# Optimization experiments

Measured on AMD Instinct MI355X. Metric: run time of the kernel, lower is better.

Reference implementation:

```python
import jax, jax.numpy as jnp
import numpy as np

HIDDEN = 4096
NUM_HEADS = 32
HEAD_DIM = HIDDEN // NUM_HEADS
B, S = 2, 2048
ROPE_BASE = 10000.0


def setup_inputs() -> dict:
    key = jax.random.key(0)
    k1, k2, k3, k4 = jax.random.split(key, 4)
    hidden_states = jax.random.normal(k1, (B, S, HIDDEN), dtype=jnp.float32)
    positions = jnp.tile(jnp.arange(S, dtype=jnp.int32)[None, :], (B, 1))
    W_qkv = jax.random.normal(k2, (HIDDEN, 3 * HIDDEN), dtype=jnp.float32) * (HIDDEN ** -0.5)
    b_qkv = jax.random.normal(k3, (3 * HIDDEN,), dtype=jnp.float32) * 0.02
    W_o = jax.random.normal(k4, (HIDDEN, HIDDEN), dtype=jnp.float32) * (HIDDEN ** -0.5)
    return {"hidden_states": hidden_states, "positions": positions,
            "W_qkv": W_qkv, "b_qkv": b_qkv, "W_o": W_o}


def _rope(x, positions):
    # x: [B, S, H, D]; GPT-NeoX style full-dim rotary (rotary_dim = head_dim)
    half = HEAD_DIM // 2
    inv_freq = 1.0 / (ROPE_BASE ** (jnp.arange(0, half, dtype=jnp.float32) * 2.0 / HEAD_DIM))
    ang = positions.astype(jnp.float32)[:, :, None] * inv_freq[None, None, :]  # [B,S,half]
    cos = jnp.cos(ang)[:, :, None, :]  # [B,S,1,half]
    sin = jnp.sin(ang)[:, :, None, :]
    x1, x2 = x[..., :half], x[..., half:]
    return jnp.concatenate([x1 * cos - x2 * sin, x2 * cos + x1 * sin], axis=-1)


def reference(hidden_states, positions, W_qkv, b_qkv, W_o):
    qkv = jnp.einsum('bsh,hk->bsk', hidden_states, W_qkv) + b_qkv
    q, k, v = jnp.split(qkv, 3, axis=-1)
    q = q.reshape(B, S, NUM_HEADS, HEAD_DIM)
    k = k.reshape(B, S, NUM_HEADS, HEAD_DIM)
    v = v.reshape(B, S, NUM_HEADS, HEAD_DIM)
    q = _rope(q, positions)
    k = _rope(k, positions)
    scale = HEAD_DIM ** -0.5
    scores = jnp.einsum('bqhd,bkhd->bhqk', q, k) * scale  # [B,H,S,S]
    causal = jnp.tril(jnp.ones((S, S), dtype=bool))
    scores = jnp.where(causal[None, None], scores, jnp.float32(-1e30))
    probs = jax.nn.softmax(scores, axis=-1)
    ctx = jnp.einsum('bhqk,bkhd->bqhd', probs, v).reshape(B, S, HIDDEN)
    return jnp.einsum('bsh,ho->bso', ctx, W_o)
```

## Files before the change

### kernel.cpp

```cpp
#include <hip/hip_runtime.h>
#include <stdint.h>

#define HID 4096
#define NHD 32
#define HD  128
#define BB  2
#define SS  2048
#define BSZ (BB*SS)
#define N3  (3*HID)

typedef __bf16 bf16x8 __attribute__((ext_vector_type(8)));
typedef __bf16 bf16x4 __attribute__((ext_vector_type(4)));
typedef float  f32x4  __attribute__((ext_vector_type(4)));

#define MFMA16(A,B,C) __builtin_amdgcn_mfma_f32_16x16x32_bf16((A),(B),(C),0,0,0)

__device__ __forceinline__ void gl_lds16(const __bf16* g, __bf16* l) {
  __builtin_amdgcn_global_load_lds(
      (__attribute__((address_space(1))) void*)g,
      (__attribute__((address_space(3))) void*)l, 16, 0, 0);
}

__global__ void cvt_bf16(const float* __restrict__ in, __bf16* __restrict__ out, int n) {
  int i = (blockIdx.x * blockDim.x + threadIdx.x) * 4;
  if (i >= n) return;
  float4 v = *(const float4*)(in + i);
  bf16x4 r;
  r[0] = (__bf16)v.x; r[1] = (__bf16)v.y; r[2] = (__bf16)v.z; r[3] = (__bf16)v.w;
  *(bf16x4*)(out + i) = r;
}

__global__ void transp_cvt(const float* __restrict__ in, __bf16* __restrict__ out,
                           int R, int C) {
  __shared__ float t[64 * 65];
  int c0 = blockIdx.x * 64, r0 = blockIdx.y * 64;
  int tx = threadIdx.x & 15, ty = threadIdx.x >> 4;
  for (int j = 0; j < 4; ++j) {
    float4 v = *(const float4*)(in + (size_t)(r0 + ty + 16 * j) * C + c0 + tx * 4);
    float* d = t + (ty + 16 * j) * 65 + tx * 4;
    d[0] = v.x; d[1] = v.y; d[2] = v.z; d[3] = v.w;
  }
  __syncthreads();
  for (int j = 0; j < 4; ++j) {
    int cc = ty + 16 * j;
    bf16x4 o4;
    for (int e = 0; e < 4; ++e) o4[e] = (__bf16)t[(tx * 4 + e) * 65 + cc];
    *(bf16x4*)(out + (size_t)(c0 + cc) * R + r0 + tx * 4) = o4;
  }
}

__global__ __launch_bounds__(256, 2) void gemm_qkv(
    const __bf16* __restrict__ A, const __bf16* __restrict__ Bt,
    const float* __restrict__ bias, const int* __restrict__ pos,
    __bf16* __restrict__ qr, __bf16* __restrict__ kr, __bf16* __restrict__ vt,
    int M, int N, int K) {
  const int TS = 146;
  __shared__ __bf16 smem[128 * TS];
  __bf16* sA = smem;
  __bf16* sB = smem + 4096;
  const int tid = threadIdx.x;
  const int wave = tid >> 6, lane = tid & 63;
  const int quad = lane >> 4, l15 = lane & 15;
  const int t = blockIdx.y * gridDim.x + blockIdx.x;
  const int grp = t / (16 * gridDim.x), rem = t % (16 * gridDim.x);
  const int m0 = (grp * 16 + (rem & 15)) * 128;
  const int n0 = (rem >> 4) * 128;
  const int wm = (wave >> 1) * 64, wn = (wave & 1) * 64;

  f32x4 acc[4][4];
  for (int i = 0; i < 4; ++i)
    for (int j = 0; j < 4; ++j)
      acc[i][j] = (f32x4){0.f, 0.f, 0.f, 0.f};

  for (int k0 = 0; k0 < K; k0 += 32) {
    __syncthreads();
    for (int i = 0; i < 2; ++i) {
      int off = tid * 16 + i * 4096;
      int r = off >> 6;
      int c = (off >> 4) & 3;
      int cs = c ^ ((r >> 1) & 3);
      gl_lds16(A  + (size_t)(m0 + r) * K + k0 + cs * 8, sA + (off >> 1));
      gl_lds16(Bt + (size_t)(n0 + r) * K + k0 + cs * 8, sB + (off >> 1));
    }
    __syncthreads();
    bf16x8 af[4], bf[4];
    for (int i = 0; i < 4; ++i) {
      int ra = wm + i * 16 + l15;
      int rb = wn + i * 16 + l15;
      af[i] = *(const bf16x8*)(sA + ra * 32 + (quad ^ ((ra >> 1) & 3)) * 8);
      bf[i] = *(const bf16x8*)(sB + rb * 32 + (quad ^ ((rb >> 1) & 3)) * 8);
    }
    for (int im = 0; im < 4; ++im)
      for (int in = 0; in < 4; ++in)
        acc[im][in] = MFMA16(af[im], bf[in], acc[im][in]);
  }

  __syncthreads();
  for (int im = 0; im < 4; ++im)
    for (int in = 0; in < 4; ++in) {
      int col = wn + in * 16 + l15;
      float bv = bias[n0 + col];
      for (int r = 0; r < 4; ++r)
        smem[(wm + im * 16 + quad * 4 + r) * TS + col] =
            (__bf16)(acc[im][in][r] + bv);
    }
  __syncthreads();

  const int reg = n0 >> 12;
  const int h   = (n0 & 4095) >> 7;
  const int b   = m0 >> 11;
  const int s0  = m0 & 2047;
  const int bh  = b * NHD + h;

  if (reg == 2) {
    __bf16* dst = vt + (size_t)bh * HD * SS;
    int l16 = tid & 15, cb = tid >> 4;
    for (int p = 0; p < 8; ++p) {
      int c = cb + 16 * p;
      bf16x8 v8;
      for (int e = 0; e < 8; ++e) v8[e] = smem[(l16 * 8 + e) * TS + c];
      *(bf16x8*)(dst + (size_t)c * SS + s0 + l16 * 8) = v8;
    }
  } else {
    __bf16* dst = (reg == 0 ? qr : kr) + (size_t)bh * SS * HD;
    const float osc = (reg == 0) ? 0.08838834764831845f : 1.0f;
    int d2 = tid & 63, rb = (tid >> 6) * 32;
    float freq = expf(-0.14391156831212787f * (float)d2);
    for (int i = 0; i < 32; ++i) {
      int r = rb + i;
      float p = (float)pos[b * SS + s0 + r];
      float sn, cs;
      sincosf(p * freq, &sn, &cs);
      float x1 = (float)smem[r * TS + d2];
      float x2 = (float)smem[r * TS + d2 + 64];
      dst[(size_t)(s0 + r) * HD + d2]      = (__bf16)((x1 * cs - x2 * sn) * osc);
      dst[(size_t)(s0 + r) * HD + d2 + 64] = (__bf16)((x2 * cs + x1 * sn) * osc);
    }
  }
}

__global__ __launch_bounds__(256, 2) void gemm_bt(
    const __bf16* __restrict__ A, const __bf16* __restrict__ Bt,
    float* __restrict__ Cout, int M, int N, int K) {
  __shared__ __bf16 sA[128 * 32];
  __shared__ __bf16 sB[128 * 32];
  const int tid = threadIdx.x;
  const int wave = tid >> 6, lane = tid & 63;
  const int quad = lane >> 4, l15 = lane & 15;
  const int t = blockIdx.y * gridDim.x + blockIdx.x;
  const int grp = t / (16 * gridDim.x), rem = t % (16 * gridDim.x);
  const int m0 = (grp * 16 + (rem & 15)) * 128;
  const int n0 = (rem >> 4) * 128;
  const int wm = (wave >> 1) * 64, wn = (wave & 1) * 64;

  f32x4 acc[4][4];
  for (int i = 0; i < 4; ++i)
    for (int j = 0; j < 4; ++j)
      acc[i][j] = (f32x4){0.f, 0.f, 0.f, 0.f};

  for (int k0 = 0; k0 < K; k0 += 32) {
    __syncthreads();
    for (int i = 0; i < 2; ++i) {
      int off = tid * 16 + i * 4096;
      int r = off >> 6;
      int c = (off >> 4) & 3;
      int cs = c ^ ((r >> 1) & 3);
      gl_lds16(A  + (size_t)(m0 + r) * K + k0 + cs * 8, sA + (off >> 1));
      gl_lds16(Bt + (size_t)(n0 + r) * K + k0 + cs * 8, sB + (off >> 1));
    }
    __syncthreads();
    bf16x8 af[4], bf[4];
    for (int i = 0; i < 4; ++i) {
      int ra = wm + i * 16 + l15;
      int rb = wn + i * 16 + l15;
      af[i] = *(const bf16x8*)(sA + ra * 32 + (quad ^ ((ra >> 1) & 3)) * 8);
      bf[i] = *(const bf16x8*)(sB + rb * 32 + (quad ^ ((rb >> 1) & 3)) * 8);
    }
    for (int im = 0; im < 4; ++im)
      for (int in = 0; in < 4; ++in)
        acc[im][in] = MFMA16(af[im], bf[in], acc[im][in]);
  }

  for (int im = 0; im < 4; ++im)
    for (int in = 0; in < 4; ++in) {
      int col = n0 + wn + in * 16 + l15;
      for (int r = 0; r < 4; ++r) {
        int row = m0 + wm + im * 16 + quad * 4 + r;
        Cout[(size_t)row * N + col] = acc[im][in][r];
      }
    }
}

__global__ __launch_bounds__(256, 2) void flash_attn(
    const __bf16* __restrict__ qr, const __bf16* __restrict__ kr,
    const __bf16* __restrict__ vt, __bf16* __restrict__ ctx) {
  __shared__ __bf16 sKP[4 * 32 * 136];
  __shared__ __bf16 sV[128 * 128];
  const int bh = blockIdx.x;
  const int qt = 15 - blockIdx.y;
  const int b = bh >> 5, h = bh & 31;
  const int tid = threadIdx.x;
  const int wave = tid >> 6, lane = tid & 63;
  const int quad = lane >> 4, l15 = lane & 15;
  const int q0 = qt * 128;

  const __bf16* qbase = qr + (size_t)bh * SS * HD;
  const __bf16* kbase = kr + (size_t)bh * SS * HD;
  const __bf16* vbase = vt + (size_t)bh * HD * SS;
  __bf16* sK = sKP;
  __bf16* pw = sKP + wave * (32 * 136);

  bf16x8 qf[2][4];
  for (int im = 0; im < 2; ++im) {
    int row = q0 + wave * 32 + im * 16 + l15;
    for (int ks = 0; ks < 4; ++ks)
      qf[im][ks] = *(const bf16x8*)(qbase + (size_t)row * HD + ks * 32 + quad * 8);
  }

  f32x4 o[2][8];
  for (int im = 0; im < 2; ++im)
    for (int jd = 0; jd < 8; ++jd)
      o[im][jd] = (f32x4){0.f, 0.f, 0.f, 0.f};
  float l_i[2][4];
  for (int im = 0; im < 2; ++im)
    for (int rg = 0; rg < 4; ++rg) l_i[im][rg] = 0.f;

  for (int kt = 0; kt <= qt; ++kt) {
    const int k0 = kt * 128;
    __syncthreads();
    for (int i = 0; i < 8; ++i) {
      int off = tid * 16 + i * 4096;
      int r  = off >> 8;
      int cl = (off >> 4) & 15;
      int cg = (cl & 8) | ((cl & 7) ^ (r & 7));
      gl_lds16(kbase + (size_t)(k0 + r) * HD + cg * 8, sK + (off >> 1));
      gl_lds16(vbase + (size_t)r * SS + k0 + cg * 8,   sV + (off >> 1));
    }
    __syncthreads();

    f32x4 s[2][8];
    for (int im = 0; im < 2; ++im)
      for (int jn = 0; jn < 8; ++jn)
        s[im][jn] = (f32x4){0.f, 0.f, 0.f, 0.f};
    for (int ks = 0; ks < 4; ++ks) {
      bf16x8 kf[8];
      for (int jn = 0; jn < 8; ++jn) {
        int row = jn * 16 + l15;
        int c = ks * 4 + quad;
        int p = (c & 8) | ((c & 7) ^ (row & 7));
        kf[jn] = *(const bf16x8*)(sK + row * 128 + p * 8);
      }
      for (int im = 0; im < 2; ++im)
        for (int jn = 0; jn < 8; ++jn)
          s[im][jn] = MFMA16(qf[im][ks], kf[jn], s[im][jn]);
    }
    __syncthreads();

    const bool diag = (kt == qt);
    for (int im = 0; im < 2; ++im)
      for (int rg = 0; rg < 4; ++rg) {
        int rowg = q0 + wave * 32 + im * 16 + quad * 4 + rg;
        float rs = 0.f;
        for (int jn = 0; jn < 8; ++jn) {
          float p = (diag && (k0 + jn * 16 + l15) > rowg)
                        ? 0.f : __expf(s[im][jn][rg]);
          s[im][jn][rg] = p;
          rs += p;
        }
        for (int d = 1; d < 16; d <<= 1) rs += __shfl_xor(rs, d);
        l_i[im][rg] += rs;
      }

    for (int im = 0; im < 2; ++im)
      for (int jn = 0; jn < 8; ++jn)
        for (int rg = 0; rg < 4; ++rg)
          pw[(im * 16 + quad * 4 + rg) * 136 + jn * 16 + l15] =
              (__bf16)s[im][jn][rg];

    for (int ks = 0; ks < 4; ++ks) {
      bf16x8 pf[2], vf[8];
      for (int im = 0; im < 2; ++im)
        pf[im] = *(const bf16x8*)(pw + (im * 16 + l15) * 136 + ks * 32 + quad * 8);
      for (int jd = 0; jd < 8; ++jd) {
        int row = jd * 16 + l15;
        int c = ks * 4 + quad;
        int p = (c & 8) | ((c & 7) ^ (row & 7));
        vf[jd] = *(const bf16x8*)(sV + row * 128 + p * 8);
      }
      for (int im = 0; im < 2; ++im)
        for (int jd = 0; jd < 8; ++jd)
          o[im][jd] = MFMA16(pf[im], vf[jd], o[im][jd]);
    }
  }

  __bf16* cb = ctx + (size_t)(b * SS) * HID + h * HD;
  for (int im = 0; im < 2; ++im)
    for (int rg = 0; rg < 4; ++rg) {
      float inv = 1.0f / l_i[im][rg];
      int row = q0 + wave * 32 + im * 16 + quad * 4 + rg;
      for (int jd = 0; jd < 8; ++jd)
        cb[(size_t)row * HID + jd * 16 + l15] = (__bf16)(o[im][jd][rg] * inv);
    }
}

extern "C" void kernel_launch(void* const* d_in, const int* in_sizes, int n_in,
                              void* d_out, int out_size, void* d_ws, size_t ws_size,
                              hipStream_t stream) {
  const float* hs   = (const float*)d_in[0];
  const int*   pos  = (const int*)d_in[1];
  const float* Wqkv = (const float*)d_in[2];
  const float* bqkv = (const float*)d_in[3];
  const float* Wo   = (const float*)d_in[4];

  char* ws = (char*)d_ws;
  const size_t M32 = 33554432;
  __bf16* hsb   = (__bf16*)(ws);
  __bf16* wqkvT = (__bf16*)(ws + M32);
  __bf16* woT   = (__bf16*)(ws + 4 * M32);
  __bf16* qr    = (__bf16*)(ws + 5 * M32);
  __bf16* kr    = (__bf16*)(ws + 6 * M32);
  __bf16* vt    = (__bf16*)(ws + 7 * M32);
  __bf16* ctx   = hsb;

  cvt_bf16<<<(BSZ * HID) / 1024, 256, 0, stream>>>(hs, hsb, BSZ * HID);
  transp_cvt<<<dim3(N3 / 64, HID / 64), 256, 0, stream>>>(Wqkv, wqkvT, HID, N3);
  transp_cvt<<<dim3(HID / 64, HID / 64), 256, 0, stream>>>(Wo, woT, HID, HID);
  gemm_qkv<<<dim3(N3 / 128, BSZ / 128), 256, 0, stream>>>(hsb, wqkvT, bqkv, pos,
                                                          qr, kr, vt, BSZ, N3, HID);
  flash_attn<<<dim3(BB * NHD, SS / 128), 256, 0, stream>>>(qr, kr, vt, ctx);
  gemm_bt<<<dim3(HID / 128, BSZ / 128), 256, 0, stream>>>(ctx, woT, (float*)d_out,
                                                          BSZ, HID, HID);
}
```

Measured before the change: 1.170 ms.

## Rewrite GEMMs as 256x256 tiles with double-buffered 8-wave pipelined core

Both projection GEMMs move from 128x128 tiles with a K-step of 32 and two syncs per step to a shared 256x256-tile core. The core uses 512 threads, K-steps of 64 and double-buffered LDS, and interleaves global-to-LDS prefetch with MFMA phases using explicit barriers, waitcnt control and setprio. The block index is remapped with a simple swizzle for L2 locality, and the QKV epilogue is adapted to the larger tile with a new LDS swizzle. This targets load latency stalls and low arithmetic intensity. The cost is 128KB of LDS per block and very high register pressure, which may cap occupancy at one block per CU despite the launch bounds.

After: 964.8 us. 1.21x faster.

```diff
diff --git a/kernel.cpp b/kernel.cpp
--- a/kernel.cpp
+++ b/kernel.cpp
@@ -20,6 +20,16 @@
       (__attribute__((address_space(1))) void*)g,
       (__attribute__((address_space(3))) void*)l, 16, 0, 0);
 }
+
+__device__ __forceinline__ void block_bar() {
+  __builtin_amdgcn_sched_barrier(0);
+  __builtin_amdgcn_s_barrier();
+  __builtin_amdgcn_sched_barrier(0);
+}
+#define LGKM0() do { asm volatile("s_waitcnt lgkmcnt(0)" ::: "memory"); \
+                     __builtin_amdgcn_sched_barrier(0); } while (0)
+#define VMC(n)  do { asm volatile("s_waitcnt vmcnt(" #n ")" ::: "memory"); \
+                     __builtin_amdgcn_sched_barrier(0); } while (0)
 
 __global__ void cvt_bf16(const float* __restrict__ in, __bf16* __restrict__ out, int n) {
   int i = (blockIdx.x * blockDim.x + threadIdx.x) * 4;
@@ -49,146 +59,248 @@
   }
 }
 
-__global__ __launch_bounds__(256, 2) void gemm_qkv(
+
+__device__ __forceinline__ void ld_a4(bf16x8 a[4][2], const __bf16* base, int row, int quad) {
+#pragma unroll
+  for (int m = 0; m < 4; ++m) {
+    const int rr = row + m * 16;
+    const int sw = rr & 7;
+#pragma unroll
+    for (int kk = 0; kk < 2; ++kk)
+      a[m][kk] = *(const bf16x8*)(base + rr * 64 + ((kk * 4 + quad) ^ sw) * 8);
+  }
+}
+__device__ __forceinline__ void ld_b2(bf16x8 b[2][2], const __bf16* base, int row, int quad) {
+#pragma unroll
+  for (int n = 0; n < 2; ++n) {
+    const int rr = row + n * 16;
+    const int sw = rr & 7;
+#pragma unroll
+    for (int kk = 0; kk < 2; ++kk)
+      b[n][kk] = *(const bf16x8*)(base + rr * 64 + ((kk * 4 + quad) ^ sw) * 8);
+  }
+}
+__device__ __forceinline__ void mma_quad(f32x4 acc[8][4], bf16x8 a[4][2],
+                                         bf16x8 b[2][2], int mh, int nh) {
+  __builtin_amdgcn_s_setprio(1);
+#pragma unroll
+  for (int m = 0; m < 4; ++m)
+#pragma unroll
+    for (int n = 0; n < 2; ++n) {
+      f32x4 c = acc[mh * 4 + m][nh * 2 + n];
+      c = MFMA16(a[m][0], b[n][0], c);
+      c = MFMA16(a[m][1], b[n][1], c);
+      acc[mh * 4 + m][nh * 2 + n] = c;
+    }
+  __builtin_amdgcn_s_setprio(0);
+}
+
+__device__ __forceinline__ void core256(const __bf16* __restrict__ Ab,
+                                        const __bf16* __restrict__ Bb,
+                                        int K, __bf16* smem, f32x4 acc[8][4]) {
+  const int tid  = threadIdx.x;
+  const int wave = tid >> 6, lane = tid & 63;
+  const int quad = lane >> 4, l15 = lane & 15;
+  const int arow = ((wave >> 2) * 64) + l15;
+  const int brow = ((wave & 3) * 32) + l15;
+  const int NKT = K >> 6, NIT = NKT >> 1;
+
+  __bf16* aBuf[2] = { smem,          smem + 16384 };
+  __bf16* bBuf[2] = { smem + 32768,  smem + 49152 };
+
+  const int off0 = tid * 16, off1 = off0 + 8192;
+  const int r0 = off0 >> 7, r1 = off1 >> 7;
+  const int sO0 = r0 * K + ((((off0 >> 4) & 7) ^ (r0 & 7)) * 8);
+  const int sO1 = r1 * K + ((((off1 >> 4) & 7) ^ (r1 & 7)) * 8);
+  const int d0 = off0 >> 1, d1 = off1 >> 1;
+
+#define STG_A(buf, half, kt) do { \
+    const __bf16* s_ = Ab + (size_t)(half) * 128 * K + (size_t)(kt) * 64; \
+    gl_lds16(s_ + sO0, aBuf[buf] + (half) * 8192 + d0); \
+    gl_lds16(s_ + sO1, aBuf[buf] + (half) * 8192 + d1); } while (0)
+#define STG_B(buf, half, kt) do { \
+    const __bf16* s_ = Bb + (size_t)(half) * 128 * K + (size_t)(kt) * 64; \
+    gl_lds16(s_ + sO0, bBuf[buf] + (half) * 8192 + d0); \
+    gl_lds16(s_ + sO1, bBuf[buf] + (half) * 8192 + d1); } while (0)
+
+  bf16x8 a_r[4][2], bn0[2][2], bn1[2][2];
+
+  STG_A(0, 0, 0); STG_B(0, 0, 0); STG_B(0, 1, 0); STG_A(0, 1, 0);
+  STG_A(1, 0, 1); STG_B(1, 0, 1); STG_B(1, 1, 1);
+  VMC(6);
+  block_bar();
+
+  for (int i = 0; i < NIT; ++i) {
+    const bool last = (i == NIT - 1);
+    const int t1 = 2 * i + 1, t2 = 2 * i + 2, t3 = 2 * i + 3;
+
+    ld_a4(a_r, aBuf[0],        arow, quad);
+    ld_b2(bn0, bBuf[0],        brow, quad);
+    STG_A(1, 1, t1);
+    block_bar(); LGKM0();
+    mma_quad(acc, a_r, bn0, 0, 0);
+    block_bar();
+
+    ld_b2(bn1, bBuf[0] + 8192, brow, quad);
+    if (!last) STG_A(0, 0, t2);
+    block_bar(); LGKM0();
+    mma_quad(acc, a_r, bn1, 0, 1);
+    block_bar();
+
+    ld_a4(a_r, aBuf[0] + 8192, arow, quad);
+    if (!last) STG_B(0, 0, t2);
+    block_bar(); LGKM0();
+    mma_quad(acc, a_r, bn1, 1, 1);
+    block_bar();
+
+    if (!last) STG_B(0, 1, t2);
+    block_bar();
+    mma_quad(acc, a_r, bn0, 1, 0);
+    if (last) { VMC(0); } else { VMC(6); }
+    block_bar();
+
+    ld_a4(a_r, aBuf[1],        arow, quad);
+    ld_b2(bn0, bBuf[1],        brow, quad);
+    if (!last) STG_A(0, 1, t2);
+    block_bar(); LGKM0();
+    mma_quad(acc, a_r, bn0, 0, 0);
+    block_bar();
+
+    ld_b2(bn1, bBuf[1] + 8192, brow, quad);
+    if (!last) STG_A(1, 0, t3);
+    block_bar(); LGKM0();
+    mma_quad(acc, a_r, bn1, 0, 1);
+    block_bar();
+
+    ld_a4(a_r, aBuf[1] + 8192, arow, quad);
+    if (!last) STG_B(1, 0, t3);
+    block_bar(); LGKM0();
+    mma_quad(acc, a_r, bn1, 1, 1);
+    block_bar();
+
+    if (!last) STG_B(1, 1, t3);
+    block_bar();
+    mma_quad(acc, a_r, bn0, 1, 0);
+    VMC(6);
+    block_bar();
+  }
+#undef STG_A
+#undef STG_B
+}
+
+__device__ __forceinline__ int eswz(int r, int c) {
+  return r * 256 + ((((c >> 3) ^ (r & 31) ^ (r >> 5)) & 31) * 8) + (c & 7);
+}
+
+__global__ __launch_bounds__(512, 2) void gemm_qkv(
     const __bf16* __restrict__ A, const __bf16* __restrict__ Bt,
     const float* __restrict__ bias, const int* __restrict__ pos,
     __bf16* __restrict__ qr, __bf16* __restrict__ kr, __bf16* __restrict__ vt,
     int M, int N, int K) {
-  const int TS = 146;
-  __shared__ __bf16 smem[128 * TS];
-  __bf16* sA = smem;
-  __bf16* sB = smem + 4096;
+  __shared__ __bf16 smem[65536];
   const int tid = threadIdx.x;
   const int wave = tid >> 6, lane = tid & 63;
   const int quad = lane >> 4, l15 = lane & 15;
-  const int t = blockIdx.y * gridDim.x + blockIdx.x;
-  const int grp = t / (16 * gridDim.x), rem = t % (16 * gridDim.x);
-  const int m0 = (grp * 16 + (rem & 15)) * 128;
-  const int n0 = (rem >> 4) * 128;
-  const int wm = (wave >> 1) * 64, wn = (wave & 1) * 64;
-
-  f32x4 acc[4][4];
-  for (int i = 0; i < 4; ++i)
-    for (int j = 0; j < 4; ++j)
-      acc[i][j] = (f32x4){0.f, 0.f, 0.f, 0.f};
-
-  for (int k0 = 0; k0 < K; k0 += 32) {
-    __syncthreads();
-    for (int i = 0; i < 2; ++i) {
-      int off = tid * 16 + i * 4096;
-      int r = off >> 6;
-      int c = (off >> 4) & 3;
-      int cs = c ^ ((r >> 1) & 3);
-      gl_lds16(A  + (size_t)(m0 + r) * K + k0 + cs * 8, sA + (off >> 1));
-      gl_lds16(Bt + (size_t)(n0 + r) * K + k0 + cs * 8, sB + (off >> 1));
-    }
-    __syncthreads();
-    bf16x8 af[4], bf[4];
-    for (int i = 0; i < 4; ++i) {
-      int ra = wm + i * 16 + l15;
-      int rb = wn + i * 16 + l15;
-      af[i] = *(const bf16x8*)(sA + ra * 32 + (quad ^ ((ra >> 1) & 3)) * 8);
-      bf[i] = *(const bf16x8*)(sB + rb * 32 + (quad ^ ((rb >> 1) & 3)) * 8);
-    }
-    for (int im = 0; im < 4; ++im)
-      for (int in = 0; in < 4; ++in)
-        acc[im][in] = MFMA16(af[im], bf[in], acc[im][in]);
-  }
-
+  const int wm = (wave >> 2) * 64, wn = (wave & 3) * 32;
+
+  const int orig = blockIdx.x;
+  const int swz = (orig & 7) * 96 + (orig >> 3);
+  const int m0 = (swz & 15) * 256;
+  const int n0 = (swz >> 4) * 256;
+
+  f32x4 acc[8][4];
+#pragma unroll
+  for (int i = 0; i < 8; ++i)
+#pragma unroll
+    for (int j = 0; j < 4; ++j) acc[i][j] = (f32x4){0.f, 0.f, 0.f, 0.f};
+
+  core256(A + (size_t)m0 * K, Bt + (size_t)n0 * K, K, smem, acc);
+
+#pragma unroll
+  for (int ni = 0; ni < 4; ++ni) {
+    const int scol = (ni >> 1) * 128 + wn + (ni & 1) * 16 + l15;
+    const float bv = bias[n0 + scol];
+#pragma unroll
+    for (int mi = 0; mi < 8; ++mi) {
+      const int rbase = (mi >> 2) * 128 + wm + (mi & 3) * 16 + quad * 4;
+#pragma unroll
+      for (int rr = 0; rr < 4; ++rr)
+        smem[eswz(rbase + rr, scol)] = (__bf16)(acc[mi][ni][rr] + bv);
+    }
+  }
   __syncthreads();
-  for (int im = 0; im < 4; ++im)
-    for (int in = 0; in < 4; ++in) {
-      int col = wn + in * 16 + l15;
-      float bv = bias[n0 + col];
-      for (int r = 0; r < 4; ++r)
-        smem[(wm + im * 16 + quad * 4 + r) * TS + col] =
-            (__bf16)(acc[im][in][r] + bv);
-    }
-  __syncthreads();
 
   const int reg = n0 >> 12;
-  const int h   = (n0 & 4095) >> 7;
+  const int h0  = (n0 & 4095) >> 7;
   const int b   = m0 >> 11;
   const int s0  = m0 & 2047;
-  const int bh  = b * NHD + h;
 
   if (reg == 2) {
-    __bf16* dst = vt + (size_t)bh * HD * SS;
-    int l16 = tid & 15, cb = tid >> 4;
-    for (int p = 0; p < 8; ++p) {
-      int c = cb + 16 * p;
+    __bf16* dst = vt + (size_t)(b * NHD + h0) * HD * SS;
+    const int sg = tid & 31, cb = tid >> 5;
+    for (int p = 0; p < 16; ++p) {
+      const int c = cb + 16 * p;
       bf16x8 v8;
-      for (int e = 0; e < 8; ++e) v8[e] = smem[(l16 * 8 + e) * TS + c];
-      *(bf16x8*)(dst + (size_t)c * SS + s0 + l16 * 8) = v8;
+#pragma unroll
+      for (int e = 0; e < 8; ++e) v8[e] = smem[eswz(sg * 8 + e, c)];
+      *(bf16x8*)(dst + (size_t)(c >> 7) * HD * SS + (size_t)(c & 127) * SS +
+                 s0 + sg * 8) = v8;
     }
   } else {
-    __bf16* dst = (reg == 0 ? qr : kr) + (size_t)bh * SS * HD;
+    __bf16* dst = (reg == 0 ? qr : kr) + (size_t)(b * NHD + h0) * SS * HD;
     const float osc = (reg == 0) ? 0.08838834764831845f : 1.0f;
-    int d2 = tid & 63, rb = (tid >> 6) * 32;
-    float freq = expf(-0.14391156831212787f * (float)d2);
+    const int d2 = tid & 63, rb = (tid >> 6) * 32;
+    const float freq = expf(-0.14391156831212787f * (float)d2);
     for (int i = 0; i < 32; ++i) {
-      int r = rb + i;
-      float p = (float)pos[b * SS + s0 + r];
+      const int r = rb + i;
+      const float p = (float)pos[b * SS + s0 + r];
       float sn, cs;
       sincosf(p * freq, &sn, &cs);
-      float x1 = (float)smem[r * TS + d2];
-      float x2 = (float)smem[r * TS + d2 + 64];
-      dst[(size_t)(s0 + r) * HD + d2]      = (__bf16)((x1 * cs - x2 * sn) * osc);
-      dst[(size_t)(s0 + r) * HD + d2 + 64] = (__bf16)((x2 * cs + x1 * sn) * osc);
-    }
-  }
-}
-
-__global__ __launch_bounds__(256, 2) void gemm_bt(
+#pragma unroll
+      for (int hs = 0; hs < 2; ++hs) {
+        const float x1 = (float)smem[eswz(r, hs * 128 + d2)];
+        const float x2 = (float)smem[eswz(r, hs * 128 + d2 + 64)];
+        __bf16* dr = dst + (size_t)hs * SS * HD + (size_t)(s0 + r) * HD;
+        dr[d2]      = (__bf16)((x1 * cs - x2 * sn) * osc);
+        dr[d2 + 64] = (__bf16)((x2 * cs + x1 * sn) * osc);
+      }
+    }
+  }
+}
+
+__global__ __launch_bounds__(512, 2) void gemm_bt(
     const __bf16* __restrict__ A, const __bf16* __restrict__ Bt,
     float* __restrict__ Cout, int M, int N, int K) {
-  __shared__ __bf16 sA[128 * 32];
-  __shared__ __bf16 sB[128 * 32];
+  __shared__ __bf16 smem[65536];
   const int tid = threadIdx.x;
   const int wave = tid >> 6, lane = tid & 63;
   const int quad = lane >> 4, l15 = lane & 15;
-  const int t = blockIdx.y * gridDim.x + blockIdx.x;
-  const int grp = t / (16 * gridDim.x), rem = t % (16 * gridDim.x);
-  const int m0 = (grp * 16 + (rem & 15)) * 128;
-  const int n0 = (rem >> 4) * 128;
-  const int wm = (wave >> 1) * 64, wn = (wave & 1) * 64;
-
-  f32x4 acc[4][4];
-  for (int i = 0; i < 4; ++i)
-    for (int j = 0; j < 4; ++j)
-      acc[i][j] = (f32x4){0.f, 0.f, 0.f, 0.f};
-
-  for (int k0 = 0; k0 < K; k0 += 32) {
-    __syncthreads();
-    for (int i = 0; i < 2; ++i) {
-      int off = tid * 16 + i * 4096;
-      int r = off >> 6;
-      int c = (off >> 4) & 3;
-      int cs = c ^ ((r >> 1) & 3);
-      gl_lds16(A  + (size_t)(m0 + r) * K + k0 + cs * 8, sA + (off >> 1));
-      gl_lds16(Bt + (size_t)(n0 + r) * K + k0 + cs * 8, sB + (off >> 1));
-    }
-    __syncthreads();
-    bf16x8 af[4], bf[4];
-    for (int i = 0; i < 4; ++i) {
-      int ra = wm + i * 16 + l15;
-      int rb = wn + i * 16 + l15;
-      af[i] = *(const bf16x8*)(sA + ra * 32 + (quad ^ ((ra >> 1) & 3)) * 8);
-      bf[i] = *(const bf16x8*)(sB + rb * 32 + (quad ^ ((rb >> 1) & 3)) * 8);
-    }
-    for (int im = 0; im < 4; ++im)
-      for (int in = 0; in < 4; ++in)
-        acc[im][in] = MFMA16(af[im], bf[in], acc[im][in]);
-  }
-
-  for (int im = 0; im < 4; ++im)
-    for (int in = 0; in < 4; ++in) {
-      int col = n0 + wn + in * 16 + l15;
-      for (int r = 0; r < 4; ++r) {
-        int row = m0 + wm + im * 16 + quad * 4 + r;
-        Cout[(size_t)row * N + col] = acc[im][in][r];
-      }
-    }
+  const int wm = (wave >> 2) * 64, wn = (wave & 3) * 32;
+
+  const int orig = blockIdx.x;
+  const int swz = (orig & 7) * 32 + (orig >> 3);
+  const int m0 = (swz & 15) * 256;
+  const int n0 = (swz >> 4) * 256;
+
+  f32x4 acc[8][4];
+#pragma unroll
+  for (int i = 0; i < 8; ++i)
+#pragma unroll
+    for (int j = 0; j < 4; ++j) acc[i][j] = (f32x4){0.f, 0.f, 0.f, 0.f};
+
+  core256(A + (size_t)m0 * K, Bt + (size_t)n0 * K, K, smem, acc);
+
+#pragma unroll
+  for (int mi = 0; mi < 8; ++mi) {
+    const int row = m0 + (mi >> 2) * 128 + wm + (mi & 3) * 16 + quad * 4;
+#pragma unroll
+    for (int ni = 0; ni < 4; ++ni) {
+      const int col = n0 + (ni >> 1) * 128 + wn + (ni & 1) * 16 + l15;
+#pragma unroll
+      for (int rr = 0; rr < 4; ++rr)
+        Cout[(size_t)(row + rr) * N + col] = acc[mi][ni][rr];
+    }
+  }
 }
 
 __global__ __launch_bounds__(256, 2) void flash_attn(
@@ -325,9 +437,8 @@
   cvt_bf16<<<(BSZ * HID) / 1024, 256, 0, stream>>>(hs, hsb, BSZ * HID);
   transp_cvt<<<dim3(N3 / 64, HID / 64), 256, 0, stream>>>(Wqkv, wqkvT, HID, N3);
   transp_cvt<<<dim3(HID / 64, HID / 64), 256, 0, stream>>>(Wo, woT, HID, HID);
-  gemm_qkv<<<dim3(N3 / 128, BSZ / 128), 256, 0, stream>>>(hsb, wqkvT, bqkv, pos,
-                                                          qr, kr, vt, BSZ, N3, HID);
+  gemm_qkv<<<768, 512, 0, stream>>>(hsb, wqkvT, bqkv, pos, qr, kr, vt,
+                                    BSZ, N3, HID);
   flash_attn<<<dim3(BB * NHD, SS / 128), 256, 0, stream>>>(qr, kr, vt, ctx);
-  gemm_bt<<<dim3(HID / 128, BSZ / 128), 256, 0, stream>>>(ctx, woT, (float*)d_out,
-                                                          BSZ, HID, HID);
-}
+  gemm_bt<<<256, 512, 0, stream>>>(ctx, woT, (float*)d_out, BSZ, HID, HID);
+}
```
